# Optimization experiments

Hardware: AMD Instinct MI355X
Metric: run time of the kernel (lower is better)

The kernel has to match this reference:

```python
import jax, jax.numpy as jnp
import numpy as np
from jax import lax

INPUT_DIM, HIDDEN, NUM_LAYERS, NUM_CLASSES = 15, 64, 2, 4
B, T = 1024, 2048


def _lstm_layer(x, w_ih, w_hh, b_ih, b_hh):
    """PyTorch-convention LSTM layer (gate order i,f,g,o). x: [B,T,D] -> [B,T,H]."""
    Bsz = x.shape[0]
    H = w_hh.shape[1]
    # precompute input contribution for all timesteps: [T,B,4H]
    xg = jnp.swapaxes(jnp.einsum('btd,gd->btg', x, w_ih) + b_ih + b_hh, 0, 1)

    def step(carry, xt):
        h, c = carry
        gates = xt + h @ w_hh.T  # [B,4H]
        i, f, g, o = jnp.split(gates, 4, axis=-1)
        i = jax.nn.sigmoid(i)
        f = jax.nn.sigmoid(f)
        g = jnp.tanh(g)
        o = jax.nn.sigmoid(o)
        c = f * c + i * g
        h = o * jnp.tanh(c)
        return (h, c), h

    init = (jnp.zeros((Bsz, H), x.dtype), jnp.zeros((Bsz, H), x.dtype))
    _, hs = lax.scan(step, init, xg)  # hs: [T,B,H]
    return jnp.swapaxes(hs, 0, 1)


def setup_inputs() -> dict:
    key = jax.random.key(0)
    ks = jax.random.split(key, 11)
    s_in = 1.0 / np.sqrt(HIDDEN)
    u = lambda k, shape: jax.random.uniform(k, shape, jnp.float32, -s_in, s_in)
    return {
        'x': jax.random.normal(ks[0], (B, T, INPUT_DIM), jnp.float32),
        'w_ih0': u(ks[1], (4 * HIDDEN, INPUT_DIM)),
        'w_hh0': u(ks[2], (4 * HIDDEN, HIDDEN)),
        'b_ih0': u(ks[3], (4 * HIDDEN,)),
        'b_hh0': u(ks[4], (4 * HIDDEN,)),
        'w_ih1': u(ks[5], (4 * HIDDEN, HIDDEN)),
        'w_hh1': u(ks[6], (4 * HIDDEN, HIDDEN)),
        'b_ih1': u(ks[7], (4 * HIDDEN,)),
        'b_hh1': u(ks[8], (4 * HIDDEN,)),
        'fc_w': u(ks[9], (NUM_CLASSES, HIDDEN)),
        'fc_b': u(ks[10], (NUM_CLASSES,)),
    }


def reference(x, w_ih0, w_hh0, b_ih0, b_hh0, w_ih1, w_hh1, b_ih1, b_hh1, fc_w, fc_b):
    h1 = _lstm_layer(x, w_ih0, w_hh0, b_ih0, b_hh0)   # [B,T,H]  (eval mode: no dropout)
    h2 = _lstm_layer(h1, w_ih1, w_hh1, b_ih1, b_hh1)  # [B,T,H]
    last = h2[:, -1, :]                               # [B,H]
    logits = last @ fc_w.T + fc_b                     # [B,C]
    return jax.nn.softmax(logits, axis=1)
```

## Files before the change

### kernel.cpp

```cpp
#include <hip/hip_runtime.h>

typedef _Float16 f16;
typedef _Float16 f16x4 __attribute__((ext_vector_type(4)));
typedef _Float16 f16x8 __attribute__((ext_vector_type(8)));
typedef float    f32x4 __attribute__((ext_vector_type(4)));

#define BATCH 1024
#define TSEQ  2048
#define DIN   15
#define HID   64
#define BT    16
#define NBLK  (BATCH / BT)
#define NT    256
#define CHUNK 16
#define NCLS  4

#define P2LOG2E 2.88539008177792681472f

#if __has_builtin(__builtin_amdgcn_exp2f)
#define EXP2(x) __builtin_amdgcn_exp2f(x)
#else
#define EXP2(x) exp2f(x)
#endif

__device__ __forceinline__ float rcp_f(float x) { return __builtin_amdgcn_rcpf(x); }
__device__ __forceinline__ float sig2 (float z) { return rcp_f(1.0f + EXP2(z)); }
__device__ __forceinline__ float tanh2(float z) { return 1.0f - 2.0f * rcp_f(1.0f + EXP2(z)); }
__device__ __forceinline__ float tanhc(float c) { return tanh2(P2LOG2E * c); }

__device__ __forceinline__ f16x8 cvt8s(const float* p, float s) {
    float4 lo = ((const float4*)p)[0];
    float4 hi = ((const float4*)p)[1];
    f16x8 r;
    r[0] = (f16)(s * lo.x); r[1] = (f16)(s * lo.y);
    r[2] = (f16)(s * lo.z); r[3] = (f16)(s * lo.w);
    r[4] = (f16)(s * hi.x); r[5] = (f16)(s * hi.y);
    r[6] = (f16)(s * hi.z); r[7] = (f16)(s * hi.w);
    return r;
}

__global__ __launch_bounds__(NT, 1)
void lstm2_b16(const float* __restrict__ x,
               const float* __restrict__ wih0, const float* __restrict__ whh0,
               const float* __restrict__ bih0, const float* __restrict__ bhh0,
               const float* __restrict__ wih1, const float* __restrict__ whh1,
               const float* __restrict__ bih1, const float* __restrict__ bhh1,
               const float* __restrict__ fcw,  const float* __restrict__ fcb,
               float* __restrict__ out)
{
    const int tid = threadIdx.x;
    const int w   = tid >> 6;
    const int l   = tid & 63;
    const int m16 = l & 15;
    const int lg  = l >> 4;
    const int bbase = blockIdx.x * BT;

    __shared__ __align__(16) f16 sx[2][CHUNK][16][16];
    __shared__ __align__(16) f16 sh[2][16][128];
    f16* sxf = &sx[0][0][0][0];

    {
        int4 zero = {0, 0, 0, 0};
        int4* z = (int4*)sx;
        #pragma unroll
        for (int i = 0; i < 4; ++i) z[tid + NT * i] = zero;
        int4* zh = (int4*)sh;
        #pragma unroll
        for (int i = 0; i < 2; ++i) zh[tid + NT * i] = zero;
    }

    f16x4 bx[4];
    f16x8 bh0[4][2];
    f16x8 bh1[4][4];
    float pb0[4], pb1[4];
    #pragma unroll
    for (int i = 0; i < 4; ++i) {
        const float gsc = (i == 2) ? P2LOG2E : -1.44269504088896340736f;
        const int n = 16 * (w + 4 * i) + m16;
        #pragma unroll
        for (int j = 0; j < 4; ++j) {
            int k = 4 * lg + j;
            bx[i][j] = (f16)((k < DIN) ? gsc * wih0[n * DIN + k] : 0.0f);
        }
        #pragma unroll
        for (int f = 0; f < 2; ++f)
            bh0[i][f] = cvt8s(whh0 + n * HID + 32 * f + 8 * lg, gsc);
        #pragma unroll
        for (int f = 0; f < 4; ++f) {
            int k0 = 32 * f + 8 * lg;
            const float* src = (k0 < HID) ? (wih1 + n * HID + k0)
                                          : (whh1 + n * HID + (k0 - HID));
            bh1[i][f] = cvt8s(src, gsc);
        }
        pb0[i] = gsc * (bih0[n] + bhh0[n]);
        pb1[i] = gsc * (bih1[n] + bhh1[n]);
    }

    const float* xb = x + (size_t)bbase * TSEQ * DIN;

    int goff[15], loff[15];
    #pragma unroll
    for (int j = 0; j < 15; ++j) {
        int idx = tid + NT * j;
        int s   = idx / 240;
        int r2  = idx - s * 240;
        int b   = r2 / 15;
        int kk  = r2 - b * 15;
        goff[j] = b * TSEQ * DIN + s * DIN + kk;
        loff[j] = (s * 16 + b) * 16 + kk;
    }

    #pragma unroll
    for (int j = 0; j < 15; ++j) {
        sxf[loff[j]]        = (f16)xb[goff[j]];
        sxf[4096 + loff[j]] = (f16)xb[goff[j] + CHUNK * DIN];
    }

    float c0r[4] = {0.f, 0.f, 0.f, 0.f};
    float c1r[4] = {0.f, 0.f, 0.f, 0.f};
    float stg[15];

    const uint rb  = (uint)(m16 * 256);
    const uint szw = ((uint)(m16 & 7)) << 4;
    const uint jb  = (uint)(2 * (16 * w + m16));

    __syncthreads();

    {
        f16x4 ax = *(const f16x4*)(sxf + ((0 * 16 + m16) << 4) + 4 * lg);
        f32x4 acc[4];
        #pragma unroll
        for (int i = 0; i < 4; ++i) {
            acc[i] = (f32x4){pb0[i], pb0[i], pb0[i], pb0[i]};
            acc[i] = __builtin_amdgcn_mfma_f32_16x16x16f16(ax, bx[i], acc[i], 0, 0, 0);
        }
        char* hw = (char*)&sh[1][0][0];
        #pragma unroll
        for (int r = 0; r < 4; ++r) {
            float i0 = sig2 (acc[0][r]);
            float g0 = tanh2(acc[2][r]);
            float o0 = sig2 (acc[3][r]);
            c0r[r] = i0 * g0;
            float h0v = o0 * tanhc(c0r[r]);
            int   b   = 4 * lg + r;
            uint  bsw = ((uint)(b & 7)) << 4;
            *(f16*)(hw + b * 256 + (jb ^ bsw)) = (f16)h0v;
        }
    }

    for (int k = 0; k < TSEQ; ++k) {
        __syncthreads();
        const int t  = k + 1;
        const int pr = t & 1;
        const int pw = k & 1;
        const int ts = t & (CHUNK - 1);

        if (ts == 0 && t + CHUNK < TSEQ) {
            const int ga = (t + CHUNK) * DIN;
            #pragma unroll
            for (int j = 0; j < 15; ++j) stg[j] = xb[goff[j] + ga];
        }
        if (ts == 8 && t > CHUNK && t + 8 < TSEQ) {
            f16* dst = sxf + ((((t >> 4) + 1) & 1) << 12);
            #pragma unroll
            for (int j = 0; j < 15; ++j) dst[loff[j]] = (f16)stg[j];
        }

        const int bxf = (t >> 4) & 1;
        f16x4 ax = *(const f16x4*)(sxf + (bxf << 12) + ((ts * 16 + m16) << 4) + 4 * lg);
        const char* hb = (const char*)&sh[pr][0][0];
        f16x8 a0 = *(const f16x8*)(hb + ((rb +       16 * lg) ^ szw));
        f16x8 a1 = *(const f16x8*)(hb + ((rb +  64 + 16 * lg) ^ szw));
        f16x8 e2 = *(const f16x8*)(hb + ((rb + 128 + 16 * lg) ^ szw));
        f16x8 e3 = *(const f16x8*)(hb + ((rb + 192 + 16 * lg) ^ szw));

        f32x4 acc[4], bcc[4];
        #pragma unroll
        for (int i = 0; i < 4; ++i) {
            acc[i] = (f32x4){pb0[i], pb0[i], pb0[i], pb0[i]};
            acc[i] = __builtin_amdgcn_mfma_f32_16x16x16f16(ax, bx[i], acc[i], 0, 0, 0);
            acc[i] = __builtin_amdgcn_mfma_f32_16x16x32_f16(a0, bh0[i][0], acc[i], 0, 0, 0);
            acc[i] = __builtin_amdgcn_mfma_f32_16x16x32_f16(a1, bh0[i][1], acc[i], 0, 0, 0);
            bcc[i] = (f32x4){pb1[i], pb1[i], pb1[i], pb1[i]};
            bcc[i] = __builtin_amdgcn_mfma_f32_16x16x32_f16(a0, bh1[i][0], bcc[i], 0, 0, 0);
            bcc[i] = __builtin_amdgcn_mfma_f32_16x16x32_f16(a1, bh1[i][1], bcc[i], 0, 0, 0);
            bcc[i] = __builtin_amdgcn_mfma_f32_16x16x32_f16(e2, bh1[i][2], bcc[i], 0, 0, 0);
            bcc[i] = __builtin_amdgcn_mfma_f32_16x16x32_f16(e3, bh1[i][3], bcc[i], 0, 0, 0);
        }

        char* hw = (char*)&sh[pw][0][0];
        #pragma unroll
        for (int r = 0; r < 4; ++r) {
            float i0 = sig2 (acc[0][r]);
            float f0 = sig2 (acc[1][r]);
            float g0 = tanh2(acc[2][r]);
            float o0 = sig2 (acc[3][r]);
            c0r[r] = f0 * c0r[r] + i0 * g0;
            float h0v = o0 * tanhc(c0r[r]);

            float i1 = sig2 (bcc[0][r]);
            float f1 = sig2 (bcc[1][r]);
            float g1 = tanh2(bcc[2][r]);
            float o1 = sig2 (bcc[3][r]);
            c1r[r] = f1 * c1r[r] + i1 * g1;
            float h1v = o1 * tanhc(c1r[r]);

            int  b   = 4 * lg + r;
            uint bsw = ((uint)(b & 7)) << 4;
            *(f16*)(hw + b * 256 + ((jb      ) ^ bsw)) = (f16)h0v;
            *(f16*)(hw + b * 256 + ((jb + 128) ^ bsw)) = (f16)h1v;
        }
    }
    __syncthreads();

    if (tid < 64) {
        const int b = tid >> 2, c = tid & 3;
        const char* h1b = (const char*)&sh[1][0][0];
        float acc = fcb[c];
        #pragma unroll
        for (int j = 0; j < HID; ++j) {
            uint off = (uint)(b * 256) + (((uint)(128 + 2 * j)) ^ (((uint)(b & 7)) << 4));
            acc += (float)(*(const f16*)(h1b + off)) * fcw[c * HID + j];
        }
        float m = fmaxf(acc, __shfl_xor(acc, 1));
        m = fmaxf(m, __shfl_xor(m, 2));
        float e = __expf(acc - m);
        float s = e + __shfl_xor(e, 1);
        s += __shfl_xor(s, 2);
        out[(bbase + b) * NCLS + c] = e * rcp_f(s);
    }
}

extern "C" void kernel_launch(void* const* d_in, const int* in_sizes, int n_in,
                              void* d_out, int out_size, void* d_ws, size_t ws_size,
                              hipStream_t stream) {
    (void)in_sizes; (void)n_in; (void)out_size; (void)d_ws; (void)ws_size;
    const float* x    = (const float*)d_in[0];
    const float* wih0 = (const float*)d_in[1];
    const float* whh0 = (const float*)d_in[2];
    const float* bih0 = (const float*)d_in[3];
    const float* bhh0 = (const float*)d_in[4];
    const float* wih1 = (const float*)d_in[5];
    const float* whh1 = (const float*)d_in[6];
    const float* bih1 = (const float*)d_in[7];
    const float* bhh1 = (const float*)d_in[8];
    const float* fcw  = (const float*)d_in[9];
    const float* fcb  = (const float*)d_in[10];
    float* out = (float*)d_out;

    lstm2_b16<<<NBLK, NT, 0, stream>>>(x, wih0, whh0, bih0, bhh0,
                                       wih1, whh1, bih1, bhh1,
                                       fcw, fcb, out);
}
```

Before: 1.866 ms.

## Shrink batch tile to 4 and redistribute gate nonlinearities via LDS

Cuts each block's batch tile from 16 to 4 rows, so the grid grows from 64 to 256 blocks and uses more of the GPU's compute units. Each block stages its MFMA gate outputs through a shared-memory buffer so the nonlinearity work (sigmoid/tanh, cell update) is spread across all 256 threads, four batch rows by both layers. This adds a second barrier and an extra LDS round trip on every timestep. The MFMA tiles stay 16 rows wide, so 12 of 16 rows are padding and wasted work.

```diff
diff --git a/kernel.cpp b/kernel.cpp
--- a/kernel.cpp
+++ b/kernel.cpp
@@ -9,13 +9,14 @@
 #define TSEQ  2048
 #define DIN   15
 #define HID   64
-#define BT    16
+#define BT    4
 #define NBLK  (BATCH / BT)
 #define NT    256
 #define CHUNK 16
 #define NCLS  4
 
 #define P2LOG2E 2.88539008177792681472f
+#define NLOG2E  -1.44269504088896340736f
 
 #if __has_builtin(__builtin_amdgcn_exp2f)
 #define EXP2(x) __builtin_amdgcn_exp2f(x)
@@ -40,13 +41,13 @@
 }
 
 __global__ __launch_bounds__(NT, 1)
-void lstm2_b16(const float* __restrict__ x,
-               const float* __restrict__ wih0, const float* __restrict__ whh0,
-               const float* __restrict__ bih0, const float* __restrict__ bhh0,
-               const float* __restrict__ wih1, const float* __restrict__ whh1,
-               const float* __restrict__ bih1, const float* __restrict__ bhh1,
-               const float* __restrict__ fcw,  const float* __restrict__ fcb,
-               float* __restrict__ out)
+void lstm2_rd(const float* __restrict__ x,
+              const float* __restrict__ wih0, const float* __restrict__ whh0,
+              const float* __restrict__ bih0, const float* __restrict__ bhh0,
+              const float* __restrict__ wih1, const float* __restrict__ whh1,
+              const float* __restrict__ bih1, const float* __restrict__ bhh1,
+              const float* __restrict__ fcw,  const float* __restrict__ fcb,
+              float* __restrict__ out)
 {
     const int tid = threadIdx.x;
     const int w   = tid >> 6;
@@ -55,8 +56,9 @@
     const int lg  = l >> 4;
     const int bbase = blockIdx.x * BT;
 
-    __shared__ __align__(16) f16 sx[2][CHUNK][16][16];
-    __shared__ __align__(16) f16 sh[2][16][128];
+    __shared__ __align__(16) f16   sx[2][CHUNK][16][16];
+    __shared__ __align__(16) f16   sh[2][16][128];
+    __shared__ __align__(16) float gbuf[2][256][4];
     f16* sxf = &sx[0][0][0][0];
 
     {
@@ -75,7 +77,7 @@
     float pb0[4], pb1[4];
     #pragma unroll
     for (int i = 0; i < 4; ++i) {
-        const float gsc = (i == 2) ? P2LOG2E : -1.44269504088896340736f;
+        const float gsc = (i == 2) ? P2LOG2E : NLOG2E;
         const int n = 16 * (w + 4 * i) + m16;
         #pragma unroll
         for (int j = 0; j < 4; ++j) {
@@ -98,58 +100,70 @@
 
     const float* xb = x + (size_t)bbase * TSEQ * DIN;
 
-    int goff[15], loff[15];
+    int goff[4], loff[4];
     #pragma unroll
-    for (int j = 0; j < 15; ++j) {
+    for (int j = 0; j < 4; ++j) {
         int idx = tid + NT * j;
-        int s   = idx / 240;
-        int r2  = idx - s * 240;
+        int s   = idx / 60;
+        int r2  = idx - s * 60;
         int b   = r2 / 15;
         int kk  = r2 - b * 15;
         goff[j] = b * TSEQ * DIN + s * DIN + kk;
         loff[j] = (s * 16 + b) * 16 + kk;
     }
+    const bool v3 = (tid < 960 - 3 * NT);
 
     #pragma unroll
-    for (int j = 0; j < 15; ++j) {
-        sxf[loff[j]]        = (f16)xb[goff[j]];
-        sxf[4096 + loff[j]] = (f16)xb[goff[j] + CHUNK * DIN];
-    }
-
-    float c0r[4] = {0.f, 0.f, 0.f, 0.f};
-    float c1r[4] = {0.f, 0.f, 0.f, 0.f};
-    float stg[15];
+    for (int j = 0; j < 4; ++j) {
+        if (j < 3 || v3) {
+            sxf[loff[j]]        = (f16)xb[goff[j]];
+            sxf[4096 + loff[j]] = (f16)xb[goff[j] + CHUNK * DIN];
+        }
+    }
+
+    const int pl = tid & 1;
+    const int pb = (tid >> 1) & 3;
+    const int pj = tid >> 3;
+    float cst[2] = {0.0f, 0.0f};
+    float stg[4];
 
     const uint rb  = (uint)(m16 * 256);
     const uint szw = ((uint)(m16 & 7)) << 4;
-    const uint jb  = (uint)(2 * (16 * w + m16));
+    const uint wsw = ((uint)pb) << 4;
 
     __syncthreads();
 
     {
-        f16x4 ax = *(const f16x4*)(sxf + ((0 * 16 + m16) << 4) + 4 * lg);
+        f16x4 ax = *(const f16x4*)(sxf + (m16 << 4) + 4 * lg);
         f32x4 acc[4];
         #pragma unroll
         for (int i = 0; i < 4; ++i) {
             acc[i] = (f32x4){pb0[i], pb0[i], pb0[i], pb0[i]};
             acc[i] = __builtin_amdgcn_mfma_f32_16x16x16f16(ax, bx[i], acc[i], 0, 0, 0);
         }
+        if (lg == 0) {
+            #pragma unroll
+            for (int i = 0; i < 4; ++i)
+                *(f32x4*)&gbuf[0][16 * (w + 4 * i) + m16][0] = acc[i];
+        }
+    }
+    __syncthreads();
+    if (pl == 0) {
         char* hw = (char*)&sh[1][0][0];
         #pragma unroll
-        for (int r = 0; r < 4; ++r) {
-            float i0 = sig2 (acc[0][r]);
-            float g0 = tanh2(acc[2][r]);
-            float o0 = sig2 (acc[3][r]);
-            c0r[r] = i0 * g0;
-            float h0v = o0 * tanhc(c0r[r]);
-            int   b   = 4 * lg + r;
-            uint  bsw = ((uint)(b & 7)) << 4;
-            *(f16*)(hw + b * 256 + (jb ^ bsw)) = (f16)h0v;
-        }
-    }
+        for (int q = 0; q < 2; ++q) {
+            int jj = pj + 32 * q;
+            float i0 = sig2 (gbuf[0][      jj][pb]);
+            float g0 = tanh2(gbuf[0][128 + jj][pb]);
+            float o0 = sig2 (gbuf[0][192 + jj][pb]);
+            cst[q] = i0 * g0;
+            float hv = o0 * tanhc(cst[q]);
+            *(f16*)(hw + pb * 256 + (((uint)(2 * jj)) ^ wsw)) = (f16)hv;
+        }
+    }
+    __syncthreads();
 
     for (int k = 0; k < TSEQ; ++k) {
-        __syncthreads();
         const int t  = k + 1;
         const int pr = t & 1;
         const int pw = k & 1;
@@ -158,12 +172,14 @@
         if (ts == 0 && t + CHUNK < TSEQ) {
             const int ga = (t + CHUNK) * DIN;
             #pragma unroll
-            for (int j = 0; j < 15; ++j) stg[j] = xb[goff[j] + ga];
+            for (int j = 0; j < 4; ++j)
+                if (j < 3 || v3) stg[j] = xb[goff[j] + ga];
         }
         if (ts == 8 && t > CHUNK && t + 8 < TSEQ) {
             f16* dst = sxf + ((((t >> 4) + 1) & 1) << 12);
             #pragma unroll
-            for (int j = 0; j < 15; ++j) dst[loff[j]] = (f16)stg[j];
+            for (int j = 0; j < 4; ++j)
+                if (j < 3 || v3) dst[loff[j]] = (f16)stg[j];
         }
 
         const int bxf = (t >> 4) & 1;
@@ -187,39 +203,39 @@
             bcc[i] = __builtin_amdgcn_mfma_f32_16x16x32_f16(e2, bh1[i][2], bcc[i], 0, 0, 0);
             bcc[i] = __builtin_amdgcn_mfma_f32_16x16x32_f16(e3, bh1[i][3], bcc[i], 0, 0, 0);
         }
+        if (lg == 0) {
+            #pragma unroll
+            for (int i = 0; i < 4; ++i) {
+                const int n = 16 * (w + 4 * i) + m16;
+                *(f32x4*)&gbuf[0][n][0] = acc[i];
+                *(f32x4*)&gbuf[1][n][0] = bcc[i];
+            }
+        }
+        __syncthreads();
 
         char* hw = (char*)&sh[pw][0][0];
         #pragma unroll
-        for (int r = 0; r < 4; ++r) {
-            float i0 = sig2 (acc[0][r]);
-            float f0 = sig2 (acc[1][r]);
-            float g0 = tanh2(acc[2][r]);
-            float o0 = sig2 (acc[3][r]);
-            c0r[r] = f0 * c0r[r] + i0 * g0;
-            float h0v = o0 * tanhc(c0r[r]);
-
-            float i1 = sig2 (bcc[0][r]);
-            float f1 = sig2 (bcc[1][r]);
-            float g1 = tanh2(bcc[2][r]);
-            float o1 = sig2 (bcc[3][r]);
-            c1r[r] = f1 * c1r[r] + i1 * g1;
-            float h1v = o1 * tanhc(c1r[r]);
-
-            int  b   = 4 * lg + r;
-            uint bsw = ((uint)(b & 7)) << 4;
-            *(f16*)(hw + b * 256 + ((jb      ) ^ bsw)) = (f16)h0v;
-            *(f16*)(hw + b * 256 + ((jb + 128) ^ bsw)) = (f16)h1v;
-        }
-    }
-    __syncthreads();
-
-    if (tid < 64) {
+        for (int q = 0; q < 2; ++q) {
+            int jj = pj + 32 * q;
+            float gi = gbuf[pl][      jj][pb];
+            float gf = gbuf[pl][ 64 + jj][pb];
+            float gg = gbuf[pl][128 + jj][pb];
+            float go = gbuf[pl][192 + jj][pb];
+            float iv = sig2(gi), fv = sig2(gf), gv = tanh2(gg), ov = sig2(go);
+            cst[q] = fv * cst[q] + iv * gv;
+            float hv = ov * tanhc(cst[q]);
+            *(f16*)(hw + pb * 256 + (((uint)(2 * (pl * 64 + jj))) ^ wsw)) = (f16)hv;
+        }
+        __syncthreads();
+    }
+
+    if (tid < BT * NCLS) {
         const int b = tid >> 2, c = tid & 3;
         const char* h1b = (const char*)&sh[1][0][0];
         float acc = fcb[c];
         #pragma unroll
         for (int j = 0; j < HID; ++j) {
-            uint off = (uint)(b * 256) + (((uint)(128 + 2 * j)) ^ (((uint)(b & 7)) << 4));
+            uint off = (uint)(b * 256) + (((uint)(128 + 2 * j)) ^ (((uint)b) << 4));
             acc += (float)(*(const f16*)(h1b + off)) * fcw[c * HID + j];
         }
         float m = fmaxf(acc, __shfl_xor(acc, 1));
@@ -248,7 +264,7 @@
     const float* fcb  = (const float*)d_in[10];
     float* out = (float*)d_out;
 
-    lstm2_b16<<<NBLK, NT, 0, stream>>>(x, wih0, whh0, bih0, bhh0,
-                                       wih1, whh1, bih1, bhh1,
-                                       fcw, fcb, out);
+    lstm2_rd<<<NBLK, NT, 0, stream>>>(x, wih0, whh0, bih0, bhh0,
+                                      wih1, whh1, bih1, bhh1,
+                                      fcw, fcb, out);
 }
```

New measurement: 1.549 ms. -17.0%, faster.
